# Performance work log

Hardware: AMD Instinct MI355X
Metric: run time of the kernel (lower is better)

Reference implementation:

```python
import jax, jax.numpy as jnp
import numpy as np

N_NODES = 1_000_000
N_EDGES = 16_000_000


def setup_inputs() -> dict:
    key = jax.random.key(0)
    ks = jax.random.split(key, 12)
    x = jax.random.normal(ks[0], (N_NODES, 3), dtype=jnp.float32)
    edge_index = jax.random.randint(ks[1], (2, N_EDGES), 0, N_NODES, dtype=jnp.int64)
    # GCNConv uses Linear(in, out, bias=False) + separate post-aggregation bias
    def lin(k, fi, fo):
        return jax.random.normal(k, (fi, fo), dtype=jnp.float32) / np.sqrt(fi)
    W1 = lin(ks[2], 3, 4); b1 = jnp.zeros((4,), jnp.float32)
    W2 = lin(ks[3], 4, 4); b2 = jnp.zeros((4,), jnp.float32)
    W3 = lin(ks[4], 4, 3); b3 = jnp.zeros((3,), jnp.float32)
    Wc = lin(ks[5], 3, 5)
    bc = jax.random.normal(ks[6], (5,), dtype=jnp.float32) * 0.01
    return {"x": x, "edge_index": edge_index, "W1": W1, "b1": b1,
            "W2": W2, "b2": b2, "W3": W3, "b3": b3, "Wc": Wc, "bc": bc}


def reference(x, edge_index, W1, b1, W2, b2, W3, b3, Wc, bc):
    N = x.shape[0]
    loop = jnp.arange(N, dtype=edge_index.dtype)
    row = jnp.concatenate([edge_index[0], loop])  # source (with self-loops)
    col = jnp.concatenate([edge_index[1], loop])  # target (with self-loops)
    # symmetric GCN normalization: deg over targets incl. self-loops
    deg = jax.ops.segment_sum(jnp.ones_like(row, dtype=x.dtype), col, num_segments=N)
    dinv = jnp.where(deg > 0, jax.lax.rsqrt(deg), 0.0)
    norm = dinv[row] * dinv[col]  # [E+N]

    def gcn_conv(h, W, b):
        h = h @ W                              # [N, F_out]
        msg = norm[:, None] * h[row]           # gather + scale, [E+N, F_out]
        agg = jax.ops.segment_sum(msg, col, num_segments=N)
        return agg + b

    h = jnp.tanh(gcn_conv(x, W1, b1))
    h = jnp.tanh(gcn_conv(h, W2, b2))
    h = jnp.tanh(gcn_conv(h, W3, b3))
    out = h @ Wc + bc
    return (out, h)
```

## Files before the change

### kernel.cpp

```cpp
#include <hip/hip_runtime.h>


#define BKT_BITS 10
#define BKT_SZ   1024
#define MAXB     1024
#define MAXK     2048
#define TILE     8192
#define HTILE    4096
#define CHUNK    32768
#define TPC      4
#define SEGC     32
#define MAXSEG   32
#define ATHR     1024
#define RECSENT  0xFFFFFFFFu

typedef int v4i __attribute__((ext_vector_type(4)));

constexpr float XD_SCALE = 4096.0f;
constexpr float HD_SCALE = 16384.0f;
constexpr int   QBIAS    = 1 << 17;

__device__ __forceinline__ short q16(float v, float s) {
    int t = __float2int_rn(v * s);
    t = max(-32767, min(32767, t));
    return (short)t;
}

__device__ __forceinline__ void ld_tile(const int* __restrict__ p, long t0, long t1,
                                        int tid, int4* dst, int sentinel) {
#pragma unroll
    for (int v = 0; v < 2; ++v) {
        long e = t0 + (long)v * HTILE + (long)tid * 4;
        if (e + 3 < t1) {
            dst[v] = *(const int4*)(p + e);
        } else {
            int* d = (int*)&dst[v];
#pragma unroll
            for (int j = 0; j < 4; ++j) d[j] = (e + j < t1) ? p[e + j] : sentinel;
        }
    }
}

__global__ __launch_bounds__(ATHR) void k_hist(const int* __restrict__ row,
                                               const int* __restrict__ col, int E,
                                               unsigned short* __restrict__ cnt16,
                                               unsigned half, int NB) {
    __shared__ unsigned lh[MAXK];
    lh[threadIdx.x] = 0u; lh[threadIdx.x + 1024] = 0u;
    __syncthreads();
    long e0 = (long)blockIdx.x * TILE;
    long e1 = e0 + TILE; if (e1 > E) e1 = E;
    int4 c4[2], r4[2];
    ld_tile(col, e0, e1, threadIdx.x, c4, -1);
    ld_tile(row, e0, e1, threadIdx.x, r4, 0);
#pragma unroll
    for (int v = 0; v < 2; ++v) {
        const int* cc = (const int*)&c4[v];
        const int* rr = (const int*)&r4[v];
#pragma unroll
        for (int j = 0; j < 4; ++j) {
            unsigned b = ((unsigned)cc[j]) >> BKT_BITS;
            if (b < (unsigned)NB) {
                unsigned key = (b << 1) | (((unsigned)rr[j] >= half) ? 1u : 0u);
                atomicAdd(&lh[key], 1u);
            }
        }
    }
    __syncthreads();
    cnt16[(size_t)blockIdx.x * MAXK + threadIdx.x] = (unsigned short)lh[threadIdx.x];
    cnt16[(size_t)blockIdx.x * MAXK + threadIdx.x + 1024] =
        (unsigned short)lh[threadIdx.x + 1024];
}

__global__ __launch_bounds__(256) void k_offA(const unsigned short* __restrict__ cnt16,
                                              int ntile, unsigned* __restrict__ psum) {
    int seg = blockIdx.x >> 3;
    int k = ((blockIdx.x & 7) << 8) + threadIdx.x;
    int tlo = seg * SEGC * TPC;
    int thi = (seg + 1) * SEGC * TPC; if (thi > ntile) thi = ntile;
    unsigned s = 0;
    for (int t = tlo; t < thi; ++t) s += cnt16[(size_t)t * MAXK + k];
    psum[(size_t)seg * MAXK + k] = s;
}

__global__ __launch_bounds__(256) void k_totB(const unsigned* __restrict__ psum, int nseg,
                                              unsigned* __restrict__ kcnt) {
    int k = blockIdx.x * blockDim.x + threadIdx.x;
    unsigned s = 0;
    for (int g = 0; g < nseg; ++g) s += psum[(size_t)g * MAXK + k];
    kcnt[k] = s;
}

__global__ __launch_bounds__(1024) void k_scan2(const unsigned* __restrict__ kcnt,
                                                unsigned* __restrict__ kpfx) {
    __shared__ unsigned tot[MAXK], pfx[MAXK];
    int t = threadIdx.x;
    tot[t] = kcnt[t]; tot[t + 1024] = kcnt[t + 1024];
    __syncthreads();
    if (t == 0) {
        unsigned run = 0;
        for (int i = 0; i < MAXK; ++i) { pfx[i] = run; run += tot[i]; }
    }
    __syncthreads();
    kpfx[t] = pfx[t]; kpfx[t + 1024] = pfx[t + 1024];
}

__global__ __launch_bounds__(1024) void k_offB(unsigned* __restrict__ psum, int nseg,
                                               const unsigned* __restrict__ kpfx) {
    for (int k = threadIdx.x; k < MAXK; k += 1024) {
        unsigned run = kpfx[k];
        for (int g = 0; g < nseg; ++g) {
            unsigned t = psum[(size_t)g * MAXK + k];
            psum[(size_t)g * MAXK + k] = run;
            run += t;
        }
    }
}

__global__ __launch_bounds__(256) void k_offC(const unsigned short* __restrict__ cnt16,
                                              int ntile,
                                              const unsigned* __restrict__ psum,
                                              unsigned* __restrict__ offs, int nblk) {
    int seg = blockIdx.x >> 3;
    int k = ((blockIdx.x & 7) << 8) + threadIdx.x;
    int clo = seg * SEGC;
    int chi = clo + SEGC; if (chi > nblk) chi = nblk;
    unsigned run = psum[(size_t)seg * MAXK + k];
    for (int c = clo; c < chi; ++c) {
        offs[(size_t)c * MAXK + k] = run;
        int tlo = c * TPC, thi = tlo + TPC; if (thi > ntile) thi = ntile;
        for (int t = tlo; t < thi; ++t) run += cnt16[(size_t)t * MAXK + k];
    }
}

__global__ __launch_bounds__(ATHR, 8) void k_place(const int* __restrict__ row,
                                                   const int* __restrict__ col, int E,
                                                   const unsigned* __restrict__ offs,
                                                   const unsigned short* __restrict__ cnt16,
                                                   unsigned* __restrict__ recbuf,
                                                   unsigned half, int NB) {
    __shared__ unsigned lo[MAXK], cnt[MAXK], sc[MAXK], pc[MAXK];
    __shared__ unsigned rec[TILE];
    __shared__ unsigned short bkt[TILE];
    int tid = threadIdx.x, lane = tid & 63, wid = tid >> 6;
    lo[tid]        = offs[(size_t)blockIdx.x * MAXK + tid];
    lo[tid + 1024] = offs[(size_t)blockIdx.x * MAXK + tid + 1024];
    long base = (long)blockIdx.x * CHUNK;
    long bend = base + CHUNK; if (bend > E) bend = E;
    int ntl = (int)((bend - base + TILE - 1) / TILE);
    int4 fc[2], fr[2];
    {
        long t1 = min(base + TILE, bend);
        ld_tile(col, base, t1, tid, fc, -1);
        ld_tile(row, base, t1, tid, fr, 0);
    }
    for (int ti = 0; ti < ntl; ++ti) {
        unsigned c0 = (unsigned)cnt16[(size_t)(blockIdx.x * TPC + ti) * MAXK + tid * 2];
        unsigned c1 = (unsigned)cnt16[(size_t)(blockIdx.x * TPC + ti) * MAXK + tid * 2 + 1];
        unsigned s = c0 + c1;
        unsigned v = s;
#pragma unroll
        for (int d = 1; d < 64; d <<= 1) {
            unsigned t = __shfl_up(v, d);
            if (lane >= d) v += t;
        }
        if (lane == 63) pc[wid] = v;
        __syncthreads();
        if (tid < 16) {
            unsigned w = pc[tid];
            unsigned iw = w;
#pragma unroll
            for (int d = 1; d < 16; d <<= 1) {
                unsigned t = __shfl_up(iw, d, 16);
                if (tid >= d) iw += t;
            }
            pc[tid] = iw - w;
        }
        __syncthreads();
        unsigned tbase = pc[wid] + (v - s);
        sc[tid * 2]     = tbase;
        sc[tid * 2 + 1] = tbase + c0;
        cnt[tid * 2]     = c0;
        cnt[tid * 2 + 1] = c1;
        __syncthreads();
        pc[tid] = 0u; pc[tid + 1024] = 0u;
        __syncthreads();
        int4 cc4[2] = {fc[0], fc[1]};
        int4 cr4[2] = {fr[0], fr[1]};
#pragma unroll
        for (int vv = 0; vv < 2; ++vv) {
            const int* cc = (const int*)&cc4[vv];
            const int* rr = (const int*)&cr4[vv];
#pragma unroll
            for (int j = 0; j < 4; ++j) {
                unsigned c = (unsigned)cc[j];
                unsigned b = c >> BKT_BITS;
                if (b >= (unsigned)NB) continue;
                unsigned r = (unsigned)rr[j];
                unsigned key = (b << 1) | ((r >= half) ? 1u : 0u);
                unsigned pos = sc[key] + atomicAdd(&pc[key], 1u);
                rec[pos] = (r << BKT_BITS) | (c & (BKT_SZ - 1));
                bkt[pos] = (unsigned short)key;
            }
        }
        __syncthreads();
        unsigned total = sc[MAXK - 1] + cnt[MAXK - 1];
        if (ti + 1 < ntl) {
            long n0 = base + (long)(ti + 1) * TILE;
            long n1 = min(n0 + TILE, bend);
            ld_tile(col, n0, n1, tid, fc, -1);
            ld_tile(row, n0, n1, tid, fr, 0);
        }
        for (unsigned t = tid; t < total; t += ATHR) {
            unsigned k = bkt[t];
            recbuf[(size_t)lo[k] + (t - sc[k])] = rec[t];
        }
        __syncthreads();
        lo[tid] += cnt[tid];
        lo[tid + 1024] += cnt[tid + 1024];
        __syncthreads();
    }
}

__global__ __launch_bounds__(ATHR) void k_bcount(const unsigned* __restrict__ recbuf,
                                                 const unsigned* __restrict__ kpfx,
                                                 const unsigned* __restrict__ kcnt,
                                                 const float* __restrict__ x,
                                                 unsigned short* __restrict__ deg,
                                                 short4* __restrict__ bufA, int N) {
    __shared__ unsigned cnt[BKT_SZ];
    int b = blockIdx.x;
    cnt[threadIdx.x] = 0u;
    __syncthreads();
#pragma unroll
    for (int h = 0; h < 2; ++h) {
        unsigned seg = ((unsigned)b << 1) | (unsigned)h;
        unsigned st = kpfx[seg], n = kcnt[seg];
        for (unsigned j = threadIdx.x; j < n; j += blockDim.x)
            atomicAdd(&cnt[recbuf[(size_t)st + j] & (BKT_SZ - 1)], 1u);
    }
    __syncthreads();
    int node = (b << BKT_BITS) + threadIdx.x;
    if (node < N) {
        unsigned short d16 = (unsigned short)cnt[threadIdx.x];
        deg[node] = d16;
        float dv = rsqrtf((float)d16 + 1.0f);
        short4 o;
        o.x = q16(dv * x[(long)node*3 + 0], XD_SCALE);
        o.y = q16(dv * x[(long)node*3 + 1], XD_SCALE);
        o.z = q16(dv * x[(long)node*3 + 2], XD_SCALE);
        o.w = 0;
        bufA[node] = o;
    }
}

template <int FIN, int FOUT, bool OUT_DINV>
__global__ __launch_bounds__(ATHR) void k_bpass(const unsigned* __restrict__ recbuf,
                                                const unsigned* __restrict__ kpfx,
                                                const unsigned* __restrict__ kcnt,
                                                const short4* __restrict__ bufIn,
                                                float inv_s,
                                                const unsigned short* __restrict__ deg,
                                                const float* __restrict__ W,
                                                const float* __restrict__ bias,
                                                short4* __restrict__ bufOut, int N) {
    __shared__ unsigned long long acc[BKT_SZ][2];
    int b = blockIdx.x;
    acc[threadIdx.x][0] = 0ull; acc[threadIdx.x][1] = 0ull;
    __syncthreads();
#pragma unroll
    for (int h = 0; h < 2; ++h) {
        unsigned seg = ((unsigned)b << 1) | (unsigned)h;
        unsigned start = kpfx[seg], n = kcnt[seg];
        unsigned lim = start + n;
        unsigned abase = start & ~3u;
        unsigned tot4 = lim - abase;
        for (unsigned j = (unsigned)threadIdx.x * 4u; j < tot4; j += ATHR * 4u) {
            unsigned idx = abase + j;
            unsigned r0, r1, r2, r3;
            if (idx >= start && idx + 4u <= lim) {
                v4i r = __builtin_nontemporal_load((const v4i*)(recbuf + idx));
                r0 = (unsigned)r.x; r1 = (unsigned)r.y;
                r2 = (unsigned)r.z; r3 = (unsigned)r.w;
            } else {
                unsigned rr[4];
#pragma unroll
                for (int k = 0; k < 4; ++k) {
                    unsigned ii = idx + (unsigned)k;
                    rr[k] = (ii >= start && ii < lim) ? recbuf[ii] : RECSENT;
                }
                r0 = rr[0]; r1 = rr[1]; r2 = rr[2]; r3 = rr[3];
            }
            short4 q0, q1, q2, q3;
            if (r0 != RECSENT) q0 = bufIn[r0 >> BKT_BITS];
            if (r1 != RECSENT) q1 = bufIn[r1 >> BKT_BITS];
            if (r2 != RECSENT) q2 = bufIn[r2 >> BKT_BITS];
            if (r3 != RECSENT) q3 = bufIn[r3 >> BKT_BITS];
#define BP_ACC(rv, qv)                                                          \
            if (rv != RECSENT) {                                                \
                unsigned nl = rv & (BKT_SZ - 1);                                \
                unsigned long long v0 =                                         \
                    ((unsigned long long)(unsigned)(qv.y + QBIAS) << 32)        \
                  |  (unsigned long long)(unsigned)(qv.x + QBIAS);              \
                atomicAdd(&acc[nl][0], v0);                                     \
                if (FIN > 2) {                                                  \
                    unsigned long long v1 =                                     \
                        ((unsigned long long)(unsigned)(qv.w + QBIAS) << 32)    \
                      |  (unsigned long long)(unsigned)(qv.z + QBIAS);          \
                    atomicAdd(&acc[nl][1], v1);                                 \
                }                                                               \
            }
            BP_ACC(r0, q0) BP_ACC(r1, q1) BP_ACC(r2, q2) BP_ACC(r3, q3)
#undef BP_ACC
        }
        __syncthreads();
    }
    int node = (b << BKT_BITS) + threadIdx.x;
    if (node >= N) return;
    int dgi = (int)deg[node];
    long long db = (long long)dgi * QBIAS;
    float dv = rsqrtf((float)dgi + 1.0f);
    short4 qs = bufIn[node];
    unsigned long long a0_ = acc[threadIdx.x][0];
    unsigned long long a1_ = acc[threadIdx.x][1];
    float s[4] = {0.f, 0.f, 0.f, 0.f};
    s[0] = (float)((long long)(unsigned)(a0_)        - db + qs.x) * inv_s;
    s[1] = (float)((long long)(unsigned)(a0_ >> 32)  - db + qs.y) * inv_s;
    if (FIN > 2) {
        s[2] = (float)((long long)(unsigned)(a1_)       - db + qs.z) * inv_s;
        s[3] = (float)((long long)(unsigned)(a1_ >> 32) - db + qs.w) * inv_s;
    }
    float o[4] = {0.f, 0.f, 0.f, 0.f};
#pragma unroll
    for (int fo = 0; fo < FOUT; ++fo) {
        float t = 0.f;
#pragma unroll
        for (int fi = 0; fi < FIN; ++fi) t += s[fi] * W[fi * FOUT + fo];
        o[fo] = tanhf(dv * t + bias[fo]);
    }
    float m = OUT_DINV ? dv : 1.0f;
    short4 outv;
    outv.x = q16(o[0] * m, HD_SCALE);
    outv.y = q16(o[1] * m, HD_SCALE);
    outv.z = (FOUT > 2) ? q16(o[2] * m, HD_SCALE) : (short)0;
    outv.w = (FOUT > 3) ? q16(o[3] * m, HD_SCALE) : (short)0;
    bufOut[node] = outv;
}

__global__ __launch_bounds__(256) void k_final(const short4* __restrict__ h3q,
                                               const float* __restrict__ Wc,
                                               const float* __restrict__ bc,
                                               float* __restrict__ out,
                                               float* __restrict__ hout, int n) {
    int i = blockIdx.x * blockDim.x + threadIdx.x;
    if (i >= n) return;
    short4 q = h3q[i];
    float h0 = (float)q.x * (1.0f / HD_SCALE);
    float h1 = (float)q.y * (1.0f / HD_SCALE);
    float h2 = (float)q.z * (1.0f / HD_SCALE);
    hout[(long)i*3 + 0] = h0;
    hout[(long)i*3 + 1] = h1;
    hout[(long)i*3 + 2] = h2;
#pragma unroll
    for (int k = 0; k < 5; ++k)
        out[(long)i*5 + k] = h0 * Wc[k] + h1 * Wc[5 + k] + h2 * Wc[10 + k] + bc[k];
}

extern "C" void kernel_launch(void* const* d_in, const int* in_sizes, int n_in,
                              void* d_out, int out_size, void* d_ws, size_t ws_size,
                              hipStream_t stream) {
    const float* x   = (const float*)d_in[0];
    const int*   ei  = (const int*)d_in[1];
    const float* W1  = (const float*)d_in[2];
    const float* b1  = (const float*)d_in[3];
    const float* W2  = (const float*)d_in[4];
    const float* b2  = (const float*)d_in[5];
    const float* W3  = (const float*)d_in[6];
    const float* b3  = (const float*)d_in[7];
    const float* Wc  = (const float*)d_in[8];
    const float* bc  = (const float*)d_in[9];

    const int N = in_sizes[0] / 3;
    const int E = in_sizes[1] / 2;
    if (N > (1 << 20)) return;
    const int* row = ei;
    const int* col = ei + E;
    const int NB = (N + BKT_SZ - 1) >> BKT_BITS;
    const int ntile = (E + TILE - 1) / TILE;
    const int nblk  = (E + CHUNK - 1) / CHUNK;
    const int nseg  = (nblk + SEGC - 1) / SEGC;
    if (nseg > MAXSEG) return;
    const unsigned half = (unsigned)(N / 2);

    float* out  = (float*)d_out;
    float* hout = (float*)d_out + (long)N * 5;

    char* w0 = (char*)d_ws;
    char* w = w0;
    short4* bufA = (short4*)w;                      w += (size_t)N * 8;
    short4* bufB = (short4*)w;                      w += (size_t)N * 8;
    unsigned short* deg = (unsigned short*)w;       w += (size_t)N * 2;
    unsigned short* cnt16 = (unsigned short*)w;     w += (size_t)ntile * MAXK * 2;
    unsigned* offs  = (unsigned*)w;                 w += (size_t)nblk * MAXK * 4;
    unsigned* psum  = (unsigned*)w;                 w += (size_t)MAXSEG * MAXK * 4;
    unsigned* kpfx  = (unsigned*)w;                 w += (size_t)MAXK * 4;
    unsigned* kcnt  = (unsigned*)w;                 w += (size_t)MAXK * 4;
    unsigned* recbuf = (unsigned*)w;                w += (size_t)E * 4;
    if ((size_t)(w - w0) + 4096 > ws_size) return;

    const int BT = 256;
    const int gN = (N + BT - 1) / BT;

    k_hist<<<ntile, ATHR, 0, stream>>>(row, col, E, cnt16, half, NB);
    k_offA<<<nseg * 8, 256, 0, stream>>>(cnt16, ntile, psum);
    k_totB<<<8, 256, 0, stream>>>(psum, nseg, kcnt);
    k_scan2<<<1, 1024, 0, stream>>>(kcnt, kpfx);
    k_offB<<<1, 1024, 0, stream>>>(psum, nseg, kpfx);
    k_offC<<<nseg * 8, 256, 0, stream>>>(cnt16, ntile, psum, offs, nblk);
    k_place<<<nblk, ATHR, 0, stream>>>(row, col, E, offs, cnt16, recbuf, half, NB);
    k_bcount<<<NB, ATHR, 0, stream>>>(recbuf, kpfx, kcnt, x, deg, bufA, N);

    k_bpass<3, 4, true><<<NB, ATHR, 0, stream>>>(recbuf, kpfx, kcnt,
        bufA, 1.0f / XD_SCALE, deg, W1, b1, bufB, N);
    k_bpass<4, 4, true><<<NB, ATHR, 0, stream>>>(recbuf, kpfx, kcnt,
        bufB, 1.0f / HD_SCALE, deg, W2, b2, bufA, N);
    k_bpass<4, 3, false><<<NB, ATHR, 0, stream>>>(recbuf, kpfx, kcnt,
        bufA, 1.0f / HD_SCALE, deg, W3, b3, bufB, N);

    k_final<<<gN, BT, 0, stream>>>(bufB, Wc, bc, out, hout, N);
}
```

Baseline: 507.7 us.

## Split each aggregation pass into two per-source-half kernels with global accumulator carry

```diff
diff --git a/kernel.cpp b/kernel.cpp
--- a/kernel.cpp
+++ b/kernel.cpp
@@ -3,7 +3,6 @@
 
 #define BKT_BITS 10
 #define BKT_SZ   1024
-#define MAXB     1024
 #define MAXK     2048
 #define TILE     8192
 #define HTILE    4096
@@ -254,7 +253,7 @@
     }
 }
 
-template <int FIN, int FOUT, bool OUT_DINV>
+template <int FIN, int FOUT, bool OUT_DINV, int PHASE>
 __global__ __launch_bounds__(ATHR) void k_bpass(const unsigned* __restrict__ recbuf,
                                                 const unsigned* __restrict__ kpfx,
                                                 const unsigned* __restrict__ kcnt,
@@ -263,59 +262,69 @@
                                                 const unsigned short* __restrict__ deg,
                                                 const float* __restrict__ W,
                                                 const float* __restrict__ bias,
-                                                short4* __restrict__ bufOut, int N) {
+                                                short4* __restrict__ bufOut,
+                                                unsigned long long* __restrict__ accg,
+                                                int N) {
     __shared__ unsigned long long acc[BKT_SZ][2];
     int b = blockIdx.x;
-    acc[threadIdx.x][0] = 0ull; acc[threadIdx.x][1] = 0ull;
-    __syncthreads();
-#pragma unroll
-    for (int h = 0; h < 2; ++h) {
-        unsigned seg = ((unsigned)b << 1) | (unsigned)h;
-        unsigned start = kpfx[seg], n = kcnt[seg];
-        unsigned lim = start + n;
-        unsigned abase = start & ~3u;
-        unsigned tot4 = lim - abase;
-        for (unsigned j = (unsigned)threadIdx.x * 4u; j < tot4; j += ATHR * 4u) {
-            unsigned idx = abase + j;
-            unsigned r0, r1, r2, r3;
-            if (idx >= start && idx + 4u <= lim) {
-                v4i r = __builtin_nontemporal_load((const v4i*)(recbuf + idx));
-                r0 = (unsigned)r.x; r1 = (unsigned)r.y;
-                r2 = (unsigned)r.z; r3 = (unsigned)r.w;
-            } else {
-                unsigned rr[4];
-#pragma unroll
-                for (int k = 0; k < 4; ++k) {
-                    unsigned ii = idx + (unsigned)k;
-                    rr[k] = (ii >= start && ii < lim) ? recbuf[ii] : RECSENT;
-                }
-                r0 = rr[0]; r1 = rr[1]; r2 = rr[2]; r3 = rr[3];
+    int nodeT = (b << BKT_BITS) + threadIdx.x;
+    if (PHASE == 2) {
+        acc[threadIdx.x][0] = accg[(size_t)nodeT * 2 + 0];
+        acc[threadIdx.x][1] = accg[(size_t)nodeT * 2 + 1];
+    } else {
+        acc[threadIdx.x][0] = 0ull; acc[threadIdx.x][1] = 0ull;
+    }
+    __syncthreads();
+    unsigned seg = ((unsigned)b << 1) | (unsigned)(PHASE - 1);
+    unsigned start = kpfx[seg], n = kcnt[seg];
+    unsigned lim = start + n;
+    unsigned abase = start & ~3u;
+    unsigned tot4 = lim - abase;
+    for (unsigned j = (unsigned)threadIdx.x * 4u; j < tot4; j += ATHR * 4u) {
+        unsigned idx = abase + j;
+        unsigned r0, r1, r2, r3;
+        if (idx >= start && idx + 4u <= lim) {
+            v4i r = __builtin_nontemporal_load((const v4i*)(recbuf + idx));
+            r0 = (unsigned)r.x; r1 = (unsigned)r.y;
+            r2 = (unsigned)r.z; r3 = (unsigned)r.w;
+        } else {
+            unsigned rr[4];
+#pragma unroll
+            for (int k = 0; k < 4; ++k) {
+                unsigned ii = idx + (unsigned)k;
+                rr[k] = (ii >= start && ii < lim) ? recbuf[ii] : RECSENT;
             }
-            short4 q0, q1, q2, q3;
-            if (r0 != RECSENT) q0 = bufIn[r0 >> BKT_BITS];
-            if (r1 != RECSENT) q1 = bufIn[r1 >> BKT_BITS];
-            if (r2 != RECSENT) q2 = bufIn[r2 >> BKT_BITS];
-            if (r3 != RECSENT) q3 = bufIn[r3 >> BKT_BITS];
+            r0 = rr[0]; r1 = rr[1]; r2 = rr[2]; r3 = rr[3];
+        }
+        short4 q0, q1, q2, q3;
+        if (r0 != RECSENT) q0 = bufIn[r0 >> BKT_BITS];
+        if (r1 != RECSENT) q1 = bufIn[r1 >> BKT_BITS];
+        if (r2 != RECSENT) q2 = bufIn[r2 >> BKT_BITS];
+        if (r3 != RECSENT) q3 = bufIn[r3 >> BKT_BITS];
 #define BP_ACC(rv, qv)                                                          \
-            if (rv != RECSENT) {                                                \
-                unsigned nl = rv & (BKT_SZ - 1);                                \
-                unsigned long long v0 =                                         \
-                    ((unsigned long long)(unsigned)(qv.y + QBIAS) << 32)        \
-                  |  (unsigned long long)(unsigned)(qv.x + QBIAS);              \
-                atomicAdd(&acc[nl][0], v0);                                     \
-                if (FIN > 2) {                                                  \
-                    unsigned long long v1 =                                     \
-                        ((unsigned long long)(unsigned)(qv.w + QBIAS) << 32)    \
-                      |  (unsigned long long)(unsigned)(qv.z + QBIAS);          \
-                    atomicAdd(&acc[nl][1], v1);                                 \
-                }                                                               \
-            }
-            BP_ACC(r0, q0) BP_ACC(r1, q1) BP_ACC(r2, q2) BP_ACC(r3, q3)
+        if (rv != RECSENT) {                                                    \
+            unsigned nl = rv & (BKT_SZ - 1);                                    \
+            unsigned long long v0 =                                             \
+                ((unsigned long long)(unsigned)(qv.y + QBIAS) << 32)            \
+              |  (unsigned long long)(unsigned)(qv.x + QBIAS);                  \
+            atomicAdd(&acc[nl][0], v0);                                         \
+            if (FIN > 2) {                                                      \
+                unsigned long long v1 =                                         \
+                    ((unsigned long long)(unsigned)(qv.w + QBIAS) << 32)        \
+                  |  (unsigned long long)(unsigned)(qv.z + QBIAS);              \
+                atomicAdd(&acc[nl][1], v1);                                     \
+            }                                                                   \
+        }
+        BP_ACC(r0, q0) BP_ACC(r1, q1) BP_ACC(r2, q2) BP_ACC(r3, q3)
 #undef BP_ACC
-        }
-        __syncthreads();
-    }
-    int node = (b << BKT_BITS) + threadIdx.x;
+    }
+    __syncthreads();
+    if (PHASE == 1) {
+        accg[(size_t)nodeT * 2 + 0] = acc[threadIdx.x][0];
+        accg[(size_t)nodeT * 2 + 1] = acc[threadIdx.x][1];
+        return;
+    }
+    int node = nodeT;
     if (node >= N) return;
     int dgi = (int)deg[node];
     long long db = (long long)dgi * QBIAS;
@@ -405,6 +414,8 @@
     unsigned* psum  = (unsigned*)w;                 w += (size_t)MAXSEG * MAXK * 4;
     unsigned* kpfx  = (unsigned*)w;                 w += (size_t)MAXK * 4;
     unsigned* kcnt  = (unsigned*)w;                 w += (size_t)MAXK * 4;
+    unsigned long long* accg = (unsigned long long*)w;
+    w += (size_t)NB * BKT_SZ * 16;
     unsigned* recbuf = (unsigned*)w;                w += (size_t)E * 4;
     if ((size_t)(w - w0) + 4096 > ws_size) return;
 
@@ -420,12 +431,16 @@
     k_place<<<nblk, ATHR, 0, stream>>>(row, col, E, offs, cnt16, recbuf, half, NB);
     k_bcount<<<NB, ATHR, 0, stream>>>(recbuf, kpfx, kcnt, x, deg, bufA, N);
 
-    k_bpass<3, 4, true><<<NB, ATHR, 0, stream>>>(recbuf, kpfx, kcnt,
-        bufA, 1.0f / XD_SCALE, deg, W1, b1, bufB, N);
-    k_bpass<4, 4, true><<<NB, ATHR, 0, stream>>>(recbuf, kpfx, kcnt,
-        bufB, 1.0f / HD_SCALE, deg, W2, b2, bufA, N);
-    k_bpass<4, 3, false><<<NB, ATHR, 0, stream>>>(recbuf, kpfx, kcnt,
-        bufA, 1.0f / HD_SCALE, deg, W3, b3, bufB, N);
+#define RUN_BPASS(FIN, FOUT, ODV, BIN, ISC, WW, BB, BOUT)                          \
+    k_bpass<FIN, FOUT, ODV, 1><<<NB, ATHR, 0, stream>>>(recbuf, kpfx, kcnt,        \
+        BIN, ISC, deg, WW, BB, BOUT, accg, N);                                     \
+    k_bpass<FIN, FOUT, ODV, 2><<<NB, ATHR, 0, stream>>>(recbuf, kpfx, kcnt,        \
+        BIN, ISC, deg, WW, BB, BOUT, accg, N);
+
+    RUN_BPASS(3, 4, true, bufA, 1.0f / XD_SCALE, W1, b1, bufB)
+    RUN_BPASS(4, 4, true, bufB, 1.0f / HD_SCALE, W2, b2, bufA)
+    RUN_BPASS(4, 3, false, bufA, 1.0f / HD_SCALE, W3, b3, bufB)
+#undef RUN_BPASS
 
     k_final<<<gN, BT, 0, stream>>>(bufB, Wc, bc, out, hout, N);
 }
```

Measured after the change: 494.9 us. 2.5% less time.
